# Kernel tuning notes

Measured on AMD Instinct MI355X. Metric: run time of the kernel, lower is better.

Reference implementation:

```python
import jax, jax.numpy as jnp
import numpy as np

N_EMBED = 2048
N_HEAD = 16
HEAD_DIM = N_EMBED // N_HEAD  # 128
BATCH, SEQ = 2, 2048


def setup_inputs() -> dict:
    key = jax.random.key(0)
    k1, k2, k3 = jax.random.split(key, 3)
    x = jax.random.normal(k1, (BATCH, SEQ, N_EMBED), dtype=jnp.float32)
    # c_attn: n_embed -> (n_head + 2) * head_dim (H query heads + 1 K head + 1 V head), no bias
    w_attn = jax.random.normal(k2, (N_EMBED, (N_HEAD + 2) * HEAD_DIM), dtype=jnp.float32) * (N_EMBED ** -0.5)
    w_out = jax.random.normal(k3, (N_EMBED, N_EMBED), dtype=jnp.float32) * (N_EMBED ** -0.5)
    return {"x": x, "w_attn": w_attn, "w_out": w_out}


def _rotate_half(t):
    # split last dim in two halves (view(..., 2, -1) semantics) and rotate
    d = t.shape[-1] // 2
    x1, x2 = t[..., :d], t[..., d:]
    return jnp.concatenate([-x2, x1], axis=-1)


def reference(x, w_attn, w_out):
    B, T, E = x.shape
    H, hd = N_HEAD, HEAD_DIM

    qkv = x @ w_attn  # (B, T, (H+2)*hd)
    q = qkv[..., : H * hd].reshape(B, T, H, hd).transpose(0, 2, 1, 3)      # (B, H, T, hd)
    k = qkv[..., H * hd : (H + 1) * hd].reshape(B, T, 1, hd).transpose(0, 2, 1, 3)  # (B, 1, T, hd)
    v = qkv[..., (H + 1) * hd :].reshape(B, T, 1, hd).transpose(0, 2, 1, 3)         # (B, 1, T, hd)

    # RoPE: pos = 10000 ** ((-2*arange(0,hd,2) - 1) / hd)  (repo's exponent)
    pos = 10000.0 ** ((-2.0 * jnp.arange(0, hd, 2, dtype=jnp.float32) - 1.0) / hd)  # (hd/2,)
    angles = jnp.arange(T, dtype=jnp.float32)[:, None] * pos[None, :]               # (T, hd/2)
    rot = jnp.concatenate([angles, angles], axis=-1)                                # (T, hd)
    cos, sin = jnp.cos(rot), jnp.sin(rot)

    q = q * cos + _rotate_half(q) * sin
    k = k * cos + _rotate_half(k) * sin

    scores = jnp.matmul(q, jnp.swapaxes(k, -1, -2)) * (hd ** -0.5)  # (B, H, T, T), KV head broadcast
    attn = jax.nn.softmax(scores, axis=-1)
    out = jnp.matmul(attn, v)                                       # (B, H, T, hd)
    out = out.transpose(0, 2, 1, 3).reshape(B, T, E)
    return out @ w_out
```

## Files before the change

kernel.cpp:

```cpp
#include <hip/hip_runtime.h>
#include <hip/hip_bf16.h>
#include <math.h>

#define BATCH 2
#define SEQ   2048
#define NEMB  2048
#define NHEAD 16
#define HD    128
#define QKV_N 2304
#define BT    (BATCH*SEQ)

typedef short bf16x8 __attribute__((ext_vector_type(8)));
typedef float f32x4  __attribute__((ext_vector_type(4)));

#define AS_GLOBAL __attribute__((address_space(1)))
#define AS_LDS    __attribute__((address_space(3)))

static __device__ __forceinline__ void load_lds16(const void* g, void* l) {
    __builtin_amdgcn_global_load_lds((const AS_GLOBAL void*)g, (AS_LDS void*)l, 16, 0, 0);
}

static __device__ __forceinline__ unsigned short f2bfu(float f) {
    __hip_bfloat16 h = __float2bfloat16(f);
    return *reinterpret_cast<unsigned short*>(&h);
}

static __device__ __forceinline__ float fexp2(float x) {
    return __builtin_amdgcn_exp2f(x);
}

__global__ __launch_bounds__(256) void cast_bf16(const float* __restrict__ in,
                                                 __hip_bfloat16* __restrict__ out) {
    int i = blockIdx.x * 256 + threadIdx.x;
    float4 a = *(const float4*)(in + (size_t)i * 8);
    float4 b = *(const float4*)(in + (size_t)i * 8 + 4);
    union { unsigned short u[8]; uint4 v; } pk;
    pk.u[0] = f2bfu(a.x); pk.u[1] = f2bfu(a.y); pk.u[2] = f2bfu(a.z); pk.u[3] = f2bfu(a.w);
    pk.u[4] = f2bfu(b.x); pk.u[5] = f2bfu(b.y); pk.u[6] = f2bfu(b.z); pk.u[7] = f2bfu(b.w);
    *(uint4*)(out + (size_t)i * 8) = pk.v;
}

__global__ __launch_bounds__(256) void trans_cast(const float* __restrict__ W, int N,
                                                  __hip_bfloat16* __restrict__ WT) {
    __shared__ float tile[64][68];
    int n0 = blockIdx.x * 64, k0 = blockIdx.y * 64;
    int tid = threadIdx.x;
#pragma unroll
    for (int i = 0; i < 4; ++i) {
        int idx = tid + i * 256;
        int r = idx >> 4, c4 = (idx & 15) << 2;
        *(float4*)&tile[r][c4] = *(const float4*)&W[(size_t)(k0 + r) * N + n0 + c4];
    }
    __syncthreads();
#pragma unroll
    for (int i = 0; i < 4; ++i) {
        int idx = tid + i * 256;
        int n = idx >> 4, kk = (idx & 15) << 2;
        ushort4 o;
        o.x = f2bfu(tile[kk + 0][n]);
        o.y = f2bfu(tile[kk + 1][n]);
        o.z = f2bfu(tile[kk + 2][n]);
        o.w = f2bfu(tile[kk + 3][n]);
        *(ushort4*)&WT[(size_t)(n0 + n) * 2048 + k0 + kk] = o;
    }
}

template <typename CT>
__global__ __launch_bounds__(256, 2) void gemm_mfma(const __hip_bfloat16* __restrict__ A, int lda,
                                                    const __hip_bfloat16* __restrict__ Bt, int ldb,
                                                    CT* __restrict__ C, int ldc, int K) {
    __shared__ __hip_bfloat16 As[128 * 64];
    __shared__ __hip_bfloat16 Bs[128 * 64];

    int bn = blockIdx.x, bm = blockIdx.y;
    int tid = threadIdx.x;
    int lane = tid & 63, w = tid >> 6;
    int l15 = lane & 15, lq = lane >> 4;
    int wm = (w >> 1) * 64, wn = (w & 1) * 64;

    const __hip_bfloat16* Ab = A + (size_t)(bm * 128) * lda;
    const __hip_bfloat16* Bb = Bt + (size_t)(bn * 128) * ldb;

    int srow[4], skc[4];
#pragma unroll
    for (int p = 0; p < 4; ++p) {
        int c = p * 256 + tid;
        srow[p] = c >> 3;
        skc[p] = (c & 7) ^ (srow[p] & 7);
    }

    f32x4 acc[4][4];
#pragma unroll
    for (int i = 0; i < 4; ++i)
#pragma unroll
        for (int j = 0; j < 4; ++j) acc[i][j] = (f32x4){0.f, 0.f, 0.f, 0.f};

    for (int k0 = 0; k0 < K; k0 += 64) {
        __syncthreads();
#pragma unroll
        for (int p = 0; p < 4; ++p) {
            int c = p * 256 + tid;
            load_lds16(Ab + (size_t)srow[p] * lda + k0 + skc[p] * 8, As + c * 8);
            load_lds16(Bb + (size_t)srow[p] * ldb + k0 + skc[p] * 8, Bs + c * 8);
        }
        __syncthreads();

#pragma unroll
        for (int kc = 0; kc < 2; ++kc) {
            bf16x8 af[4], bf[4];
#pragma unroll
            for (int t = 0; t < 4; ++t) {
                int ma = wm + t * 16 + l15;
                af[t] = *(const bf16x8*)&As[(ma * 8 + ((kc * 4 + lq) ^ (ma & 7))) * 8];
                int nb = wn + t * 16 + l15;
                bf[t] = *(const bf16x8*)&Bs[(nb * 8 + ((kc * 4 + lq) ^ (nb & 7))) * 8];
            }
#pragma unroll
            for (int i = 0; i < 4; ++i)
#pragma unroll
                for (int j = 0; j < 4; ++j)
                    acc[i][j] = __builtin_amdgcn_mfma_f32_16x16x32_bf16(af[i], bf[j], acc[i][j], 0, 0, 0);
        }
    }

    int row0 = bm * 128 + wm, col0 = bn * 128 + wn;
#pragma unroll
    for (int i = 0; i < 4; ++i)
#pragma unroll
        for (int j = 0; j < 4; ++j)
#pragma unroll
            for (int r = 0; r < 4; ++r) {
                int row = row0 + i * 16 + lq * 4 + r;
                int col = col0 + j * 16 + l15;
                float v = acc[i][j][r];
                if constexpr (__is_same(CT, float)) {
                    C[(size_t)row * ldc + col] = v;
                } else {
                    C[(size_t)row * ldc + col] = __float2bfloat16(v);
                }
            }
}

__global__ __launch_bounds__(256) void rope_qk(__hip_bfloat16* __restrict__ qkv) {
    int idx = blockIdx.x * 256 + threadIdx.x;
    int d = idx & 63;
    int rest = idx >> 6;
    int slot = rest % 17;
    int row = rest / 17;
    int t = row & (SEQ - 1);

    float fr = fexp2(-13.287712379549449f * (4.0f * d + 1.0f) * (1.0f / 128.0f)) *
               0.15915494309189535f;
    float rev = (float)t * fr;
    float red = rev - floorf(rev);
    float sn = __builtin_amdgcn_sinf(red);
    float cs = __builtin_amdgcn_cosf(red);

    __hip_bfloat16* p = qkv + (size_t)row * QKV_N + slot * HD + d;
    float x1 = __bfloat162float(p[0]);
    float x2 = __bfloat162float(p[64]);
    p[0]  = __float2bfloat16(x1 * cs - x2 * sn);
    p[64] = __float2bfloat16(x2 * cs + x1 * sn);
}

__global__ __launch_bounds__(256) void transpose_v(const __hip_bfloat16* __restrict__ qkv,
                                                   __hip_bfloat16* __restrict__ vT) {
    __shared__ unsigned short tile[64][72];
    int tt = blockIdx.x, dd = blockIdx.y, b = blockIdx.z;
    int tid = threadIdx.x;
#pragma unroll
    for (int i = 0; i < 4; ++i) {
        int idx = tid + i * 256;
        int r = idx >> 4, c4 = (idx & 15) << 2;
        *(ushort4*)&tile[r][c4] = *(const ushort4*)&qkv[(size_t)(b * SEQ + tt * 64 + r) * QKV_N +
                                                        (NHEAD + 1) * HD + dd * 64 + c4];
    }
    __syncthreads();
#pragma unroll
    for (int i = 0; i < 4; ++i) {
        int idx = tid + i * 256;
        int dl = idx >> 4, t4 = (idx & 15) << 2;
        ushort4 o;
        o.x = tile[t4 + 0][dl];
        o.y = tile[t4 + 1][dl];
        o.z = tile[t4 + 2][dl];
        o.w = tile[t4 + 3][dl];
        *(ushort4*)&vT[(size_t)(b * HD + dd * 64 + dl) * SEQ + tt * 64 + t4] = o;
    }
}

__global__ __launch_bounds__(256, 2) void attn_mfma(__hip_bfloat16* __restrict__ qkv,
                                                    const __hip_bfloat16* __restrict__ vT) {
    int qt = blockIdx.x;
    int h  = blockIdx.y;
    int b  = blockIdx.z;
    int tid  = threadIdx.x;
    int w    = tid >> 6;
    int lane = tid & 63;
    int l15  = lane & 15;
    int lq   = lane >> 4;
    int l7   = l15 & 7;

    __shared__ __hip_bfloat16 Ks[64 * 128];
    __shared__ __hip_bfloat16 Vt[128 * 64];
    __shared__ __hip_bfloat16 Ps[4][32 * 64];

    int qrow0 = b * SEQ + qt * 128 + w * 32;
    bf16x8 qf[2][4];
#pragma unroll
    for (int qb2 = 0; qb2 < 2; ++qb2)
#pragma unroll
        for (int kc = 0; kc < 4; ++kc)
            qf[qb2][kc] = *(const bf16x8*)&qkv[(size_t)(qrow0 + qb2 * 16 + l15) * QKV_N +
                                              h * HD + kc * 32 + lq * 8];

    f32x4 of[2][8];
#pragma unroll
    for (int qb2 = 0; qb2 < 2; ++qb2)
#pragma unroll
        for (int db = 0; db < 8; ++db) of[qb2][db] = (f32x4){0.f, 0.f, 0.f, 0.f};
    float l_st[2] = {0.f, 0.f};

    const size_t kbase = (size_t)b * SEQ * QKV_N + NHEAD * HD;
    const size_t vbase = (size_t)b * HD * SEQ;
    const float sl2e = 0.08838834764831845f * 1.4426950408889634f;
    const float MFIX = 16.0f;

    for (int kt = 0; kt < SEQ / 64; ++kt) {
        __syncthreads();
#pragma unroll
        for (int i = 0; i < 4; ++i) {
            int c = tid + i * 256;
            int r = c >> 4, sc = (c & 15) ^ (r & 15);
            load_lds16(&qkv[kbase + (size_t)(kt * 64 + r) * QKV_N + sc * 8], &Ks[c * 8]);
        }
#pragma unroll
        for (int i = 0; i < 4; ++i) {
            int c = tid + i * 256;
            int d = c >> 3, sc = (c & 7) ^ (d & 7);
            load_lds16(&vT[vbase + (size_t)d * SEQ + kt * 64 + sc * 8], &Vt[c * 8]);
        }
        __syncthreads();

        f32x4 sf[4][2];
#pragma unroll
        for (int kb = 0; kb < 4; ++kb) {
            bf16x8 kf[4];
#pragma unroll
            for (int kc = 0; kc < 4; ++kc)
                kf[kc] = *(const bf16x8*)&Ks[((kb * 16 + l15) * 16 + ((kc * 4 + lq) ^ l15)) * 8];
#pragma unroll
            for (int qb2 = 0; qb2 < 2; ++qb2) {
                f32x4 acc = (f32x4){0.f, 0.f, 0.f, 0.f};
#pragma unroll
                for (int kc = 0; kc < 4; ++kc)
                    acc = __builtin_amdgcn_mfma_f32_16x16x32_bf16(kf[kc], qf[qb2][kc], acc, 0, 0, 0);
                sf[kb][qb2] = acc;
            }
        }

#pragma unroll
        for (int qb2 = 0; qb2 < 2; ++qb2) {
            float sum = 0.f;
            int qr = qb2 * 16 + l15;
#pragma unroll
            for (int kb = 0; kb < 4; ++kb) {
                float p0 = fexp2(fmaf(sf[kb][qb2][0], sl2e, -MFIX));
                float p1 = fexp2(fmaf(sf[kb][qb2][1], sl2e, -MFIX));
                float p2 = fexp2(fmaf(sf[kb][qb2][2], sl2e, -MFIX));
                float p3 = fexp2(fmaf(sf[kb][qb2][3], sl2e, -MFIX));
                sum += (p0 + p1) + (p2 + p3);
                ushort4 pk;
                pk.x = f2bfu(p0); pk.y = f2bfu(p1); pk.z = f2bfu(p2); pk.w = f2bfu(p3);
                int cc = (kb * 2 + (lq >> 1)) ^ l7;
                *(ushort4*)&Ps[w][(qr * 8 + cc) * 8 + (lq & 1) * 4] = pk;
            }
            l_st[qb2] += sum;
        }

#pragma unroll
        for (int kc2 = 0; kc2 < 2; ++kc2) {
            bf16x8 pa[2];
#pragma unroll
            for (int qb2 = 0; qb2 < 2; ++qb2)
                pa[qb2] = *(const bf16x8*)&Ps[w][((qb2 * 16 + l15) * 8 +
                                                 ((kc2 * 4 + lq) ^ l7)) * 8];
#pragma unroll
            for (int db = 0; db < 8; ++db) {
                bf16x8 vb = *(const bf16x8*)&Vt[((db * 16 + l15) * 8 +
                                                ((kc2 * 4 + lq) ^ l7)) * 8];
#pragma unroll
                for (int qb2 = 0; qb2 < 2; ++qb2)
                    of[qb2][db] = __builtin_amdgcn_mfma_f32_16x16x32_bf16(pa[qb2], vb, of[qb2][db], 0, 0, 0);
            }
        }
    }

    float i_t[2][4];
#pragma unroll
    for (int qb2 = 0; qb2 < 2; ++qb2) {
        float l = l_st[qb2];
        l += __shfl_xor(l, 16, 64);
        l += __shfl_xor(l, 32, 64);
        float inv = 1.0f / l;
#pragma unroll
        for (int r = 0; r < 4; ++r) i_t[qb2][r] = __shfl(inv, lq * 4 + r, 64);
    }
#pragma unroll
    for (int qb2 = 0; qb2 < 2; ++qb2)
#pragma unroll
        for (int db = 0; db < 8; ++db)
#pragma unroll
            for (int r = 0; r < 4; ++r) {
                float v = of[qb2][db][r] * i_t[qb2][r];
                qkv[(size_t)(qrow0 + qb2 * 16 + lq * 4 + r) * QKV_N + h * HD + db * 16 + l15] =
                    __float2bfloat16(v);
            }
}

extern "C" void kernel_launch(void* const* d_in, const int* in_sizes, int n_in,
                              void* d_out, int out_size, void* d_ws, size_t ws_size,
                              hipStream_t stream) {
    const float* x      = (const float*)d_in[0];
    const float* w_attn = (const float*)d_in[1];
    const float* w_out  = (const float*)d_in[2];
    float* out = (float*)d_out;

    char* ws = (char*)d_ws;
    __hip_bfloat16* qkvb = (__hip_bfloat16*)ws;
    __hip_bfloat16* wT   = (__hip_bfloat16*)(ws + 18874368);
    __hip_bfloat16* vT   = (__hip_bfloat16*)(ws + 28311552);
    __hip_bfloat16* xb   = (__hip_bfloat16*)d_out;

    cast_bf16<<<(BT * NEMB / 8) / 256, 256, 0, stream>>>(x, xb);
    trans_cast<<<dim3(QKV_N / 64, NEMB / 64), 256, 0, stream>>>(w_attn, QKV_N, wT);

    gemm_mfma<__hip_bfloat16><<<dim3(QKV_N / 128, BT / 128), 256, 0, stream>>>(
        xb, NEMB, wT, NEMB, qkvb, QKV_N, NEMB);

    rope_qk<<<(BT * 17 * 64) / 256, 256, 0, stream>>>(qkvb);

    transpose_v<<<dim3(SEQ / 64, HD / 64, BATCH), 256, 0, stream>>>(qkvb, vT);

    attn_mfma<<<dim3(SEQ / 128, NHEAD, BATCH), 256, 0, stream>>>(qkvb, vT);

    trans_cast<<<dim3(NEMB / 64, NEMB / 64), 256, 0, stream>>>(w_out, NEMB, wT);
    gemm_mfma<float><<<dim3(NEMB / 128, BT / 128), 256, 0, stream>>>(
        qkvb, QKV_N, wT, NEMB, out, NEMB, NEMB);
}
```

Measured before the change: 281.7 us.

## Fuse RoPE into QKV GEMM epilogue via permuted weights; double attention KV tile

The w_attn columns are permuted during transpose-cast so each warp's accumulator tiles hold matching RoPE half-pairs. Rotation is then applied in the QKV GEMM epilogue, which removes the separate rope_qk read-modify-write pass over Q/K. The attention kernel now loads 128 keys per iteration instead of 64, halving the number of barrier/load rounds. The cost is doubled K/V LDS (64KB total plus P buffers), which may cut occupancy below two blocks per CU. The permuted output layout must stay consistent with the downstream attention dot products.

```diff
diff --git a/kernel.cpp b/kernel.cpp
--- a/kernel.cpp
+++ b/kernel.cpp
@@ -40,6 +40,7 @@
     *(uint4*)(out + (size_t)i * 8) = pk.v;
 }
 
+template <bool PERM>
 __global__ __launch_bounds__(256) void trans_cast(const float* __restrict__ W, int N,
                                                   __hip_bfloat16* __restrict__ WT) {
     __shared__ float tile[64][68];
@@ -49,7 +50,20 @@
     for (int i = 0; i < 4; ++i) {
         int idx = tid + i * 256;
         int r = idx >> 4, c4 = (idx & 15) << 2;
-        *(float4*)&tile[r][c4] = *(const float4*)&W[(size_t)(k0 + r) * N + n0 + c4];
+        int np = n0 + c4;
+        int src;
+        if constexpr (PERM) {
+            int slot = np >> 7, p = np & 127;
+            if (slot < 17) {
+                int g = p >> 5, half = (p >> 4) & 1, m = p & 15;
+                src = slot * 128 + half * 64 + g * 16 + m;
+            } else {
+                src = np;
+            }
+        } else {
+            src = np;
+        }
+        *(float4*)&tile[r][c4] = *(const float4*)&W[(size_t)(k0 + r) * N + src];
     }
     __syncthreads();
 #pragma unroll
@@ -65,7 +79,7 @@
     }
 }
 
-template <typename CT>
+template <typename CT, bool ROPE>
 __global__ __launch_bounds__(256, 2) void gemm_mfma(const __hip_bfloat16* __restrict__ A, int lda,
                                                     const __hip_bfloat16* __restrict__ Bt, int ldb,
                                                     CT* __restrict__ C, int ldc, int K) {
@@ -124,6 +138,39 @@
     }
 
     int row0 = bm * 128 + wm, col0 = bn * 128 + wn;
+
+    if constexpr (ROPE) {
+        if (bn < 17) {
+            float fr[2];
+#pragma unroll
+            for (int jh = 0; jh < 2; ++jh) {
+                int g = (wn >> 5) + jh;
+                float dlow = (float)(g * 16 + l15);
+                fr[jh] = fexp2(-13.287712379549449f * (4.0f * dlow + 1.0f) * (1.0f / 128.0f)) *
+                         0.15915494309189535f;
+            }
+#pragma unroll
+            for (int i = 0; i < 4; ++i)
+#pragma unroll
+                for (int r = 0; r < 4; ++r) {
+                    int row = row0 + i * 16 + lq * 4 + r;
+                    float tpos = (float)(row & (SEQ - 1));
+#pragma unroll
+                    for (int jh = 0; jh < 2; ++jh) {
+                        int j = jh * 2;
+                        float rev = tpos * fr[jh];
+                        float red = rev - floorf(rev);
+                        float sn = __builtin_amdgcn_sinf(red);
+                        float cs = __builtin_amdgcn_cosf(red);
+                        float x1 = acc[i][j][r];
+                        float x2 = acc[i][j + 1][r];
+                        acc[i][j][r]     = x1 * cs - x2 * sn;
+                        acc[i][j + 1][r] = x2 * cs + x1 * sn;
+                    }
+                }
+        }
+    }
+
 #pragma unroll
     for (int i = 0; i < 4; ++i)
 #pragma unroll
@@ -139,28 +186,6 @@
                     C[(size_t)row * ldc + col] = __float2bfloat16(v);
                 }
             }
-}
-
-__global__ __launch_bounds__(256) void rope_qk(__hip_bfloat16* __restrict__ qkv) {
-    int idx = blockIdx.x * 256 + threadIdx.x;
-    int d = idx & 63;
-    int rest = idx >> 6;
-    int slot = rest % 17;
-    int row = rest / 17;
-    int t = row & (SEQ - 1);
-
-    float fr = fexp2(-13.287712379549449f * (4.0f * d + 1.0f) * (1.0f / 128.0f)) *
-               0.15915494309189535f;
-    float rev = (float)t * fr;
-    float red = rev - floorf(rev);
-    float sn = __builtin_amdgcn_sinf(red);
-    float cs = __builtin_amdgcn_cosf(red);
-
-    __hip_bfloat16* p = qkv + (size_t)row * QKV_N + slot * HD + d;
-    float x1 = __bfloat162float(p[0]);
-    float x2 = __bfloat162float(p[64]);
-    p[0]  = __float2bfloat16(x1 * cs - x2 * sn);
-    p[64] = __float2bfloat16(x2 * cs + x1 * sn);
 }
 
 __global__ __launch_bounds__(256) void transpose_v(const __hip_bfloat16* __restrict__ qkv,
@@ -201,8 +226,8 @@
     int lq   = lane >> 4;
     int l7   = l15 & 7;
 
-    __shared__ __hip_bfloat16 Ks[64 * 128];
-    __shared__ __hip_bfloat16 Vt[128 * 64];
+    __shared__ __hip_bfloat16 Ks[128 * 128];
+    __shared__ __hip_bfloat16 Vt[128 * 128];
     __shared__ __hip_bfloat16 Ps[4][32 * 64];
 
     int qrow0 = b * SEQ + qt * 128 + w * 32;
@@ -226,72 +251,77 @@
     const float sl2e = 0.08838834764831845f * 1.4426950408889634f;
     const float MFIX = 16.0f;
 
-    for (int kt = 0; kt < SEQ / 64; ++kt) {
+    for (int kt = 0; kt < SEQ / 128; ++kt) {
         __syncthreads();
 #pragma unroll
-        for (int i = 0; i < 4; ++i) {
+        for (int i = 0; i < 8; ++i) {
             int c = tid + i * 256;
             int r = c >> 4, sc = (c & 15) ^ (r & 15);
-            load_lds16(&qkv[kbase + (size_t)(kt * 64 + r) * QKV_N + sc * 8], &Ks[c * 8]);
-        }
-#pragma unroll
-        for (int i = 0; i < 4; ++i) {
+            load_lds16(&qkv[kbase + (size_t)(kt * 128 + r) * QKV_N + sc * 8], &Ks[c * 8]);
+        }
+#pragma unroll
+        for (int i = 0; i < 8; ++i) {
             int c = tid + i * 256;
-            int d = c >> 3, sc = (c & 7) ^ (d & 7);
-            load_lds16(&vT[vbase + (size_t)d * SEQ + kt * 64 + sc * 8], &Vt[c * 8]);
+            int d = c >> 4, sc = (c & 15) ^ (d & 15);
+            load_lds16(&vT[vbase + (size_t)d * SEQ + kt * 128 + sc * 8], &Vt[c * 8]);
         }
         __syncthreads();
 
-        f32x4 sf[4][2];
-#pragma unroll
-        for (int kb = 0; kb < 4; ++kb) {
-            bf16x8 kf[4];
-#pragma unroll
-            for (int kc = 0; kc < 4; ++kc)
-                kf[kc] = *(const bf16x8*)&Ks[((kb * 16 + l15) * 16 + ((kc * 4 + lq) ^ l15)) * 8];
+#pragma unroll
+        for (int half = 0; half < 2; ++half) {
+            f32x4 sf[4][2];
+#pragma unroll
+            for (int kb = 0; kb < 4; ++kb) {
+                int krow = half * 64 + kb * 16 + l15;
+                bf16x8 kf[4];
+#pragma unroll
+                for (int kc = 0; kc < 4; ++kc)
+                    kf[kc] = *(const bf16x8*)&Ks[(krow * 16 + ((kc * 4 + lq) ^ l15)) * 8];
+#pragma unroll
+                for (int qb2 = 0; qb2 < 2; ++qb2) {
+                    f32x4 acc = (f32x4){0.f, 0.f, 0.f, 0.f};
+#pragma unroll
+                    for (int kc = 0; kc < 4; ++kc)
+                        acc = __builtin_amdgcn_mfma_f32_16x16x32_bf16(kf[kc], qf[qb2][kc], acc, 0, 0, 0);
+                    sf[kb][qb2] = acc;
+                }
+            }
+
 #pragma unroll
             for (int qb2 = 0; qb2 < 2; ++qb2) {
-                f32x4 acc = (f32x4){0.f, 0.f, 0.f, 0.f};
-#pragma unroll
-                for (int kc = 0; kc < 4; ++kc)
-                    acc = __builtin_amdgcn_mfma_f32_16x16x32_bf16(kf[kc], qf[qb2][kc], acc, 0, 0, 0);
-                sf[kb][qb2] = acc;
-            }
-        }
-
-#pragma unroll
-        for (int qb2 = 0; qb2 < 2; ++qb2) {
-            float sum = 0.f;
-            int qr = qb2 * 16 + l15;
-#pragma unroll
-            for (int kb = 0; kb < 4; ++kb) {
-                float p0 = fexp2(fmaf(sf[kb][qb2][0], sl2e, -MFIX));
-                float p1 = fexp2(fmaf(sf[kb][qb2][1], sl2e, -MFIX));
-                float p2 = fexp2(fmaf(sf[kb][qb2][2], sl2e, -MFIX));
-                float p3 = fexp2(fmaf(sf[kb][qb2][3], sl2e, -MFIX));
-                sum += (p0 + p1) + (p2 + p3);
-                ushort4 pk;
-                pk.x = f2bfu(p0); pk.y = f2bfu(p1); pk.z = f2bfu(p2); pk.w = f2bfu(p3);
-                int cc = (kb * 2 + (lq >> 1)) ^ l7;
-                *(ushort4*)&Ps[w][(qr * 8 + cc) * 8 + (lq & 1) * 4] = pk;
-            }
-            l_st[qb2] += sum;
-        }
-
-#pragma unroll
-        for (int kc2 = 0; kc2 < 2; ++kc2) {
-            bf16x8 pa[2];
-#pragma unroll
-            for (int qb2 = 0; qb2 < 2; ++qb2)
-                pa[qb2] = *(const bf16x8*)&Ps[w][((qb2 * 16 + l15) * 8 +
-                                                 ((kc2 * 4 + lq) ^ l7)) * 8];
-#pragma unroll
-            for (int db = 0; db < 8; ++db) {
-                bf16x8 vb = *(const bf16x8*)&Vt[((db * 16 + l15) * 8 +
-                                                ((kc2 * 4 + lq) ^ l7)) * 8];
+                float sum = 0.f;
+                int qr = qb2 * 16 + l15;
+#pragma unroll
+                for (int kb = 0; kb < 4; ++kb) {
+                    float p0 = fexp2(fmaf(sf[kb][qb2][0], sl2e, -MFIX));
+                    float p1 = fexp2(fmaf(sf[kb][qb2][1], sl2e, -MFIX));
+                    float p2 = fexp2(fmaf(sf[kb][qb2][2], sl2e, -MFIX));
+                    float p3 = fexp2(fmaf(sf[kb][qb2][3], sl2e, -MFIX));
+                    sum += (p0 + p1) + (p2 + p3);
+                    ushort4 pk;
+                    pk.x = f2bfu(p0); pk.y = f2bfu(p1); pk.z = f2bfu(p2); pk.w = f2bfu(p3);
+                    int cc = (kb * 2 + (lq >> 1)) ^ l7;
+                    *(ushort4*)&Ps[w][(qr * 8 + cc) * 8 + (lq & 1) * 4] = pk;
+                }
+                l_st[qb2] += sum;
+            }
+
+#pragma unroll
+            for (int kc2 = 0; kc2 < 2; ++kc2) {
+                bf16x8 pa[2];
 #pragma unroll
                 for (int qb2 = 0; qb2 < 2; ++qb2)
-                    of[qb2][db] = __builtin_amdgcn_mfma_f32_16x16x32_bf16(pa[qb2], vb, of[qb2][db], 0, 0, 0);
+                    pa[qb2] = *(const bf16x8*)&Ps[w][((qb2 * 16 + l15) * 8 +
+                                                     ((kc2 * 4 + lq) ^ l7)) * 8];
+#pragma unroll
+                for (int db = 0; db < 8; ++db) {
+                    int drow = db * 16 + l15;
+                    bf16x8 vb = *(const bf16x8*)&Vt[(drow * 16 +
+                                                    ((half * 8 + kc2 * 4 + lq) ^ l15)) * 8];
+#pragma unroll
+                    for (int qb2 = 0; qb2 < 2; ++qb2)
+                        of[qb2][db] = __builtin_amdgcn_mfma_f32_16x16x32_bf16(pa[qb2], vb, of[qb2][db], 0, 0, 0);
+                }
             }
         }
     }
@@ -333,18 +363,16 @@
     __hip_bfloat16* xb   = (__hip_bfloat16*)d_out;
 
     cast_bf16<<<(BT * NEMB / 8) / 256, 256, 0, stream>>>(x, xb);
-    trans_cast<<<dim3(QKV_N / 64, NEMB / 64), 256, 0, stream>>>(w_attn, QKV_N, wT);
-
-    gemm_mfma<__hip_bfloat16><<<dim3(QKV_N / 128, BT / 128), 256, 0, stream>>>(
+    trans_cast<true><<<dim3(QKV_N / 64, NEMB / 64), 256, 0, stream>>>(w_attn, QKV_N, wT);
+
+    gemm_mfma<__hip_bfloat16, true><<<dim3(QKV_N / 128, BT / 128), 256, 0, stream>>>(
         xb, NEMB, wT, NEMB, qkvb, QKV_N, NEMB);
 
-    rope_qk<<<(BT * 17 * 64) / 256, 256, 0, stream>>>(qkvb);
-
     transpose_v<<<dim3(SEQ / 64, HD / 64, BATCH), 256, 0, stream>>>(qkvb, vT);
 
     attn_mfma<<<dim3(SEQ / 128, NHEAD, BATCH), 256, 0, stream>>>(qkvb, vT);
 
-    trans_cast<<<dim3(NEMB / 64, NEMB / 64), 256, 0, stream>>>(w_out, NEMB, wT);
-    gemm_mfma<float><<<dim3(NEMB / 128, BT / 128), 256, 0, stream>>>(
+    trans_cast<false><<<dim3(NEMB / 64, NEMB / 64), 256, 0, stream>>>(w_out, NEMB, wT);
+    gemm_mfma<float, false><<<dim3(NEMB / 128, BT / 128), 256, 0, stream>>>(
         qkvb, QKV_N, wT, NEMB, out, NEMB, NEMB);
 }
```

Result: slower. 308.3 us (+9.4%).
